# Optimization experiments

Hardware: AMD Instinct MI355X
Metric: run time of the kernel (lower is better)

## Reference

```python
import jax, jax.numpy as jnp
import numpy as np

N = 8192   # number of sentences/layout elements
D = 1024   # matrix_dim = nlp.output_dim (768) + position.output_dim (256)
E = 8192   # number of relation rows (cv_relation)
K = 16     # 1 center + 15 neighbors per row


def setup_inputs() -> dict:
    key = jax.random.key(0)
    k1, k2, k3 = jax.random.split(key, 3)
    sent_feat = jax.random.normal(k1, (N, D), dtype=jnp.float32)
    # nn.Linear(2D -> 1): weight vector W [2D] and bias b [1]
    W = jax.random.normal(k2, (2 * D,), dtype=jnp.float32) * 0.02
    b = jnp.zeros((1,), dtype=jnp.float32)
    edge = jax.random.randint(k3, (E, K), 0, N)  # cv_relation indices
    return {"sent_feat": sent_feat, "W": W, "b": b, "edge": edge}


def reference(sent_feat, W, b, edge):
    d = sent_feat.shape[-1]
    # Linear([x_i ; x_j]) @ W + b == x_i @ w1 + x_j @ w2 + b  (exact same math,
    # avoids materializing the [.., 2D] concat and the NxNx2D all-pairs tensor)
    w1, w2 = W[:d], W[d:]

    # pair_score: gather center/neighbors then score each (center, neighbor) pair
    lookup = sent_feat[edge]                      # [E, K, D]
    center = lookup[:, 0]                         # [E, D]
    neighbors = lookup[:, 1:]                     # [E, K-1, D]
    pair_score = (center @ w1)[:, None] + neighbors @ w2 + b   # [E, K-1]

    # all_score: dense all-pairs score matrix over all N sentences
    s1 = sent_feat @ w1                           # [N]
    s2 = sent_feat @ w2                           # [N]
    all_score = s1[:, None] + s2[None, :] + b     # [N, N]

    return pair_score, all_score
```

## Files before the change

### kernel.cpp

```cpp
#include <hip/hip_runtime.h>

#define NROWS 8192
#define DDIM  1024
#define EEDGE 8192
#define KNB   16

typedef float f32x4 __attribute__((ext_vector_type(4)));

__global__ __launch_bounds__(256) void dots_kernel(const float* __restrict__ sent,
                                                   const float* __restrict__ W,
                                                   const float* __restrict__ b,
                                                   float* __restrict__ s1,
                                                   float* __restrict__ s2) {
    int gwave = (blockIdx.x * 256 + threadIdx.x) >> 6;
    int lane  = threadIdx.x & 63;
    if (gwave >= NROWS) return;
    const f32x4* row = reinterpret_cast<const f32x4*>(sent + (size_t)gwave * DDIM);
    const f32x4* w1v = reinterpret_cast<const f32x4*>(W);
    const f32x4* w2v = reinterpret_cast<const f32x4*>(W + DDIM);
    float a1 = 0.f, a2 = 0.f;
#pragma unroll
    for (int it = 0; it < 4; ++it) {
        int idx = lane + it * 64;
        f32x4 r  = __builtin_nontemporal_load(&row[idx]);
        f32x4 x1 = w1v[idx];
        f32x4 x2 = w2v[idx];
        a1 += r.x * x1.x + r.y * x1.y + r.z * x1.z + r.w * x1.w;
        a2 += r.x * x2.x + r.y * x2.y + r.z * x2.z + r.w * x2.w;
    }
#pragma unroll
    for (int off = 32; off > 0; off >>= 1) {
        a1 += __shfl_xor(a1, off, 64);
        a2 += __shfl_xor(a2, off, 64);
    }
    if (lane == 0) {
        s1[gwave] = a1 + b[0];
        s2[gwave] = a2;
    }
}

__global__ __launch_bounds__(256) void fused_kernel(const int* __restrict__ edge,
                                                    const float* __restrict__ s1,
                                                    const float* __restrict__ s2,
                                                    float* __restrict__ pair,
                                                    float* __restrict__ alls) {
    int row = blockIdx.x;
    int t   = threadIdx.x;

    if (t < KNB - 1) {
        int c = edge[row * KNB];
        int n = edge[row * KNB + 1 + t];
        pair[row * (KNB - 1) + t] = s1[c] + s2[n];
    }

    float v1 = s1[row];
    const f32x4* s2v = reinterpret_cast<const f32x4*>(s2);
    f32x4* o = reinterpret_cast<f32x4*>(alls + (size_t)row * NROWS);
#pragma unroll
    for (int it = 0; it < 8; ++it) {
        int j = t + it * 256;
        f32x4 v = s2v[j];
        f32x4 r = v + v1;
        __builtin_nontemporal_store(r, &o[j]);
    }
}

extern "C" void kernel_launch(void* const* d_in, const int* in_sizes, int n_in,
                              void* d_out, int out_size, void* d_ws, size_t ws_size,
                              hipStream_t stream) {
    const float* sent = (const float*)d_in[0];
    const float* W    = (const float*)d_in[1];
    const float* b    = (const float*)d_in[2];
    const int*   edge = (const int*)  d_in[3];

    float* out  = (float*)d_out;
    float* pair = out;
    float* alls = out + (size_t)EEDGE * (KNB - 1);

    float* s1 = (float*)d_ws;
    float* s2 = s1 + NROWS;

    dots_kernel<<<NROWS / 4, 256, 0, stream>>>(sent, W, b, s1, s2);
    fused_kernel<<<NROWS, 256, 0, stream>>>(edge, s1, s2, pair, alls);
}
```

Measured before the change: 59.94 us.

## Switch all-pairs writer to persistent grid-stride kernel with plain stores

Replaces the one-block-per-row writer with a fixed grid of 512 blocks. Each thread keeps a single s2 column vector in registers and grid-strides over the flattened output, reading s1 per row. The pair-score work is redistributed at 16 edges per block. Nontemporal loads and stores are replaced by ordinary ones. The aim is to cut block launch overhead and repeated s2 loads, at the cost of lower occupancy and of losing streaming-store cache hints on a write-bound output.

```diff
diff --git a/kernel.cpp b/kernel.cpp
--- a/kernel.cpp
+++ b/kernel.cpp
@@ -4,6 +4,10 @@
 #define DDIM  1024
 #define EEDGE 8192
 #define KNB   16
+
+#define GSBLK 512
+#define TOTV  (NROWS * (NROWS / 4))
+#define NITER (TOTV / (GSBLK * 256))
 
 typedef float f32x4 __attribute__((ext_vector_type(4)));
 
@@ -22,7 +26,7 @@
 #pragma unroll
     for (int it = 0; it < 4; ++it) {
         int idx = lane + it * 64;
-        f32x4 r  = __builtin_nontemporal_load(&row[idx]);
+        f32x4 r  = row[idx];
         f32x4 x1 = w1v[idx];
         f32x4 x2 = w2v[idx];
         a1 += r.x * x1.x + r.y * x1.y + r.z * x1.z + r.w * x1.w;
@@ -39,29 +43,36 @@
     }
 }
 
-__global__ __launch_bounds__(256) void fused_kernel(const int* __restrict__ edge,
+__global__ __launch_bounds__(256) void write_kernel(const int* __restrict__ edge,
                                                     const float* __restrict__ s1,
                                                     const float* __restrict__ s2,
                                                     float* __restrict__ pair,
                                                     float* __restrict__ alls) {
-    int row = blockIdx.x;
-    int t   = threadIdx.x;
+    const int t  = threadIdx.x;
+    const int gt = blockIdx.x * 256 + t;
 
-    if (t < KNB - 1) {
-        int c = edge[row * KNB];
-        int n = edge[row * KNB + 1 + t];
-        pair[row * (KNB - 1) + t] = s1[c] + s2[n];
+    if (t < 16 * (KNB - 1)) {
+        int e = blockIdx.x * 16 + t / (KNB - 1);
+        int k = t % (KNB - 1);
+        int c = edge[e * KNB];
+        int n = edge[e * KNB + 1 + k];
+        pair[e * (KNB - 1) + k] = s1[c] + s2[n];
     }
 
-    float v1 = s1[row];
     const f32x4* s2v = reinterpret_cast<const f32x4*>(s2);
-    f32x4* o = reinterpret_cast<f32x4*>(alls + (size_t)row * NROWS);
+    f32x4* ov = reinterpret_cast<f32x4*>(alls);
+
+    const float v2x4[4] = { s2v[gt & 2047].x, s2v[gt & 2047].y,
+                            s2v[gt & 2047].z, s2v[gt & 2047].w };
+    f32x4 v2;
+    v2.x = v2x4[0]; v2.y = v2x4[1]; v2.z = v2x4[2]; v2.w = v2x4[3];
+
 #pragma unroll
-    for (int it = 0; it < 8; ++it) {
-        int j = t + it * 256;
-        f32x4 v = s2v[j];
-        f32x4 r = v + v1;
-        __builtin_nontemporal_store(r, &o[j]);
+    for (int it = 0; it < NITER; ++it) {
+        int g   = gt + it * (GSBLK * 256);
+        int row = g >> 11;
+        f32x4 v = v2 + s1[row];
+        ov[g] = v;
     }
 }
 
@@ -81,5 +92,5 @@
     float* s2 = s1 + NROWS;
 
     dots_kernel<<<NROWS / 4, 256, 0, stream>>>(sent, W, b, s1, s2);
-    fused_kernel<<<NROWS, 256, 0, stream>>>(edge, s1, s2, pair, alls);
+    write_kernel<<<GSBLK, 256, 0, stream>>>(edge, s1, s2, pair, alls);
 }
```

After: 57.33 us. -4.3%, faster.
